# Performance work log

Measured on AMD Instinct MI355X. Metric: run time of the kernel, lower is better.

## Reference

```python
import jax, jax.numpy as jnp
import numpy as np

EMBED_DIM = 128
NUM_HEADS = 16
D_K = EMBED_DIM // NUM_HEADS  # n_wires per head = 8
DEPTH = 1
DIM = 2 ** D_K  # 256 state amplitudes


def _cnot_chain_inverse_perm(d, depth):
    """Inverse permutation of basis states under `depth` rounds of the CNOT ladder
    CNOT(0,1),...,CNOT(d-2,d-1),CNOT(d-1,0). Wire 0 = most significant bit."""
    idx = np.arange(2 ** d)
    shifts = d - 1 - np.arange(d)
    bits = (idx[:, None] >> shifts) & 1  # (2^d, d)
    for _ in range(depth):
        for w in range(d - 1):
            bits[:, w + 1] ^= bits[:, w]
        bits[:, 0] ^= bits[:, d - 1]
    fwd = (bits << shifts).sum(axis=1)  # psi'[fwd[b]] = psi[b]
    inv = np.empty_like(fwd)
    inv[fwd] = idx  # psi'[j] = psi[inv[j]]
    return inv


def _pauliz_signs(d):
    idx = np.arange(2 ** d)
    shifts = d - 1 - np.arange(d)
    bits = (idx[:, None] >> shifts) & 1
    return (1.0 - 2.0 * bits).astype(np.float32)  # (2^d, d)


_INV_PERM = jnp.asarray(_cnot_chain_inverse_perm(D_K, DEPTH))
_SIGNS = jnp.asarray(_pauliz_signs(D_K))


def quantum_head(angles):
    """angles: (..., d) RX rotation angles. Returns PauliZ expectations (..., d).

    Product state amplitudes after per-wire RX from |0..0>: probabilities are
    products of cos^2/sin^2; CNOT ladder is a basis permutation; <Z_w> is a
    signed sum of probabilities."""
    half = angles * 0.5
    c2 = jnp.cos(half) ** 2
    s2 = jnp.sin(half) ** 2
    lead = angles.shape[:-1]
    p = jnp.ones(lead + (1,), angles.dtype)
    for w in range(D_K):  # builds (..., 2^d) probability vector
        pair = jnp.stack([c2[..., w], s2[..., w]], axis=-1)
        p = (p[..., :, None] * pair[..., None, :]).reshape(lead + (-1,))
    p = p[..., _INV_PERM]  # apply CNOT ladder permutation
    return p @ _SIGNS  # (..., d) PauliZ expectations


def setup_inputs() -> dict:
    key = jax.random.key(0)
    ks = jax.random.split(key, 10)
    B, S, E = 8, 512, EMBED_DIM
    sc = 1.0 / np.sqrt(E)
    return {
        "x": jax.random.normal(ks[0], (B, S, E), jnp.float32),
        "Wq": jax.random.normal(ks[1], (E, E), jnp.float32) * sc,
        "bq": jnp.zeros((E,), jnp.float32),
        "Wk": jax.random.normal(ks[2], (E, E), jnp.float32) * sc,
        "bk": jnp.zeros((E,), jnp.float32),
        "Wv": jax.random.normal(ks[3], (E, E), jnp.float32) * sc,
        "bv": jnp.zeros((E,), jnp.float32),
        "Wo": jax.random.normal(ks[4], (E, E), jnp.float32) * sc,
        "bo": jnp.zeros((E,), jnp.float32),
        "theta": jax.random.normal(ks[5], (NUM_HEADS, D_K), jnp.float32),
    }


def reference(x, Wq, bq, Wk, bk, Wv, bv, Wo, bo, theta):
    B, S, E = x.shape
    H, dk = NUM_HEADS, D_K

    def split_heads(y):  # (B,S,E) -> (B,H,S,dk)
        return y.reshape(B, S, H, dk).transpose(0, 2, 1, 3)

    q = split_heads(x @ Wq + bq)
    k = split_heads(x @ Wk + bk)
    v = split_heads(x @ Wv + bv)

    th = theta[None, :, None, :]  # broadcast per-head trainable RX angles
    qh = quantum_head(q + th)
    kh = quantum_head(k + th)
    vh = quantum_head(v + th)

    scores = jnp.einsum("bhsd,bhtd->bhst", qh, kh) / jnp.sqrt(jnp.asarray(dk, x.dtype))
    attn = jax.nn.softmax(scores, axis=-1)
    out = jnp.einsum("bhst,bhtd->bhsd", attn, vh)
    out = out.transpose(0, 2, 1, 3).reshape(B, S, E)
    return out @ Wo + bo
```

## Files before the change

kernel.cpp:

```cpp
#include <hip/hip_runtime.h>
#include <hip/hip_bf16.h>
#include <math.h>

#define BB 8
#define SS 512
#define EE 128
#define HH 16
#define DKK 8

#define FMA4(ACC, S, W) do { (ACC).x += (S)*(W).x; (ACC).y += (S)*(W).y; \
                             (ACC).z += (S)*(W).z; (ACC).w += (S)*(W).w; } while(0)
#define DOT4(A, B) ((A).x*(B).x + (A).y*(B).y + (A).z*(B).z + (A).w*(B).w)

__global__ __launch_bounds__(256, 4) void k_qkvq(
    const float* __restrict__ x,
    const float* __restrict__ Wq, const float* __restrict__ bq,
    const float* __restrict__ Wk, const float* __restrict__ bk,
    const float* __restrict__ Wv, const float* __restrict__ bv,
    const float* __restrict__ theta,
    float* __restrict__ qh, float* __restrict__ kh, float* __restrict__ vh)
{
    __shared__ float xs[16][128];
    const int t = threadIdx.x;
    const int m = blockIdx.y;
    const int row0 = blockIdx.x * 16;

    {
        const float4* xv = (const float4*)(x + (size_t)row0 * 128);
        float4* xsv = (float4*)&xs[0][0];
        xsv[t]       = xv[t];
        xsv[t + 256] = xv[t + 256];
    }
    __syncthreads();

    const int cg   = t & 31;
    const int col0 = cg * 4;
    const int rg   = t >> 5;
    const int r0   = rg * 2;

    const float* __restrict__ W  = (m == 0) ? Wq : (m == 1) ? Wk : Wv;
    const float* __restrict__ bb = (m == 0) ? bq : (m == 1) ? bk : bv;
    float* __restrict__ outp     = (m == 0) ? qh : (m == 1) ? kh : vh;

    float4 acc0 = *(const float4*)&bb[col0];
    float4 acc1 = acc0;

    #pragma unroll 4
    for (int k4 = 0; k4 < 32; ++k4) {
        const float4 xa = ((const float4*)xs[r0 + 0])[k4];
        const float4 xb = ((const float4*)xs[r0 + 1])[k4];
        const float4 w0 = *(const float4*)&W[(k4 * 4 + 0) * 128 + col0];
        const float4 w1 = *(const float4*)&W[(k4 * 4 + 1) * 128 + col0];
        const float4 w2 = *(const float4*)&W[(k4 * 4 + 2) * 128 + col0];
        const float4 w3 = *(const float4*)&W[(k4 * 4 + 3) * 128 + col0];
        FMA4(acc0, xa.x, w0); FMA4(acc0, xa.y, w1);
        FMA4(acc0, xa.z, w2); FMA4(acc0, xa.w, w3);
        FMA4(acc1, xb.x, w0); FMA4(acc1, xb.y, w1);
        FMA4(acc1, xb.z, w2); FMA4(acc1, xb.w, w3);
    }

    const float4 th = *(const float4*)&theta[col0];
    const int h    = cg >> 1;
    const int half = cg & 1;

    float4 accs[2] = {acc0, acc1};
    #pragma unroll
    for (int r = 0; r < 2; ++r) {
        float4 c;
        c.x = __cosf(accs[r].x + th.x);
        c.y = __cosf(accs[r].y + th.y);
        c.z = __cosf(accs[r].z + th.z);
        c.w = __cosf(accs[r].w + th.w);
        const float p0 = c.x;
        const float p1 = p0 * c.y;
        const float p2 = p1 * c.z;
        const float p3 = p2 * c.w;
        const float recv = __shfl_xor(p3, 1);
        float4 o;
        if (half == 0) {
            const float s123 = c.y * c.z * c.w;
            o.x = s123 * recv;
            o.y = p1;
            o.z = p2;
            o.w = p3;
        } else {
            o.x = recv * p0;
            o.y = recv * p1;
            o.z = recv * p2;
            o.w = recv * p3;
        }
        const int g  = row0 + r0 + r;
        const int b_ = g >> 9;
        const int s  = g & 511;
        *(float4*)&outp[(((size_t)b_ * HH + h) * SS + s) * DKK + half * 4] = o;
    }
}

__global__ __launch_bounds__(512, 4) void k_attn(
    const float* __restrict__ qh, const float* __restrict__ kh,
    const float* __restrict__ vh, float* __restrict__ hid)
{
    __shared__ float4 smem[3072];
    float4* kk = smem;
    float4* vv = smem + 1024;

    const int t  = threadIdx.x;
    const int L  = t & 63;
    const int wv = t >> 6;
    const int bh = blockIdx.x & 127;
    const int q0 = (blockIdx.x >> 7) * 256;

    {
        const float4* kg = (const float4*)kh + (size_t)bh * 1024;
        const float4* vg = (const float4*)vh + (size_t)bh * 1024;
        kk[t]       = kg[t];
        kk[t + 512] = kg[t + 512];
        vv[t]       = vg[t];
        vv[t + 512] = vg[t + 512];
    }

    const float scale = 0.35355339059327373f;
    float4 qa[4], qb[4];
    {
        const float4* qg = (const float4*)qh + ((size_t)bh * 512 + q0) * 2;
        #pragma unroll
        for (int r = 0; r < 4; ++r) {
            float4 a = qg[(L + 64 * r) * 2];
            float4 b = qg[(L + 64 * r) * 2 + 1];
            a.x *= scale; a.y *= scale; a.z *= scale; a.w *= scale;
            b.x *= scale; b.y *= scale; b.z *= scale; b.w *= scale;
            qa[r] = a; qb[r] = b;
        }
    }
    __syncthreads();

    float4 aA[4], aB[4];
    float  den[4];
    #pragma unroll
    for (int r = 0; r < 4; ++r) {
        aA[r] = make_float4(0.f, 0.f, 0.f, 0.f);
        aB[r] = make_float4(0.f, 0.f, 0.f, 0.f);
        den[r] = 0.f;
    }

    const float4* kbase = kk + wv * 128;
    const float4* vbase = vv + wv * 128;

    #pragma unroll 4
    for (int j = 0; j < 64; ++j) {
        const float4 k0 = kbase[2 * j];
        const float4 k1 = kbase[2 * j + 1];
        const float4 v0 = vbase[2 * j];
        const float4 v1 = vbase[2 * j + 1];
        #pragma unroll
        for (int r = 0; r < 4; ++r) {
            const float s = DOT4(qa[r], k0) + DOT4(qb[r], k1);
            const float e = __expf(s);
            den[r] += e;
            FMA4(aA[r], e, v0);
            FMA4(aB[r], e, v1);
        }
    }

    __syncthreads();

    float4* part = smem;
    if (wv < 4) {
        #pragma unroll
        for (int r = 0; r < 4; ++r) {
            const int idx = (wv * 256 + L + 64 * r) * 3;
            part[idx]     = aA[r];
            part[idx + 1] = aB[r];
            part[idx + 2] = make_float4(den[r], 0.f, 0.f, 0.f);
        }
    }
    __syncthreads();
    if (wv >= 4) {
        #pragma unroll
        for (int r = 0; r < 4; ++r) {
            const int idx = ((wv - 4) * 256 + L + 64 * r) * 3;
            float4 pa = part[idx];
            float4 pb = part[idx + 1];
            float4 pd = part[idx + 2];
            pa.x += aA[r].x; pa.y += aA[r].y; pa.z += aA[r].z; pa.w += aA[r].w;
            pb.x += aB[r].x; pb.y += aB[r].y; pb.z += aB[r].z; pb.w += aB[r].w;
            pd.x += den[r];
            part[idx]     = pa;
            part[idx + 1] = pb;
            part[idx + 2] = pd;
        }
    }
    __syncthreads();

    if (t < 256) {
        float4 rA = make_float4(0.f, 0.f, 0.f, 0.f), rB = rA;
        float rd = 0.f;
        #pragma unroll
        for (int w = 0; w < 4; ++w) {
            const int idx = (w * 256 + t) * 3;
            const float4 a = part[idx];
            const float4 b = part[idx + 1];
            rA.x += a.x; rA.y += a.y; rA.z += a.z; rA.w += a.w;
            rB.x += b.x; rB.y += b.y; rB.z += b.z; rB.w += b.w;
            rd   += part[idx + 2].x;
        }
        const float inv = 1.0f / rd;
        rA.x *= inv; rA.y *= inv; rA.z *= inv; rA.w *= inv;
        rB.x *= inv; rB.y *= inv; rB.z *= inv; rB.w *= inv;
        const int b_ = bh >> 4, h = bh & 15;
        float* o = hid + ((size_t)(b_ * 512) + q0 + t) * 128 + h * 8;
        ((float4*)o)[0] = rA;
        ((float4*)o)[1] = rB;
    }
}

__global__ __launch_bounds__(256, 4) void k_out(
    const float* __restrict__ hid, const float* __restrict__ Wo,
    const float* __restrict__ bo, float* __restrict__ out)
{
    __shared__ float hs[16][128];
    const int t = threadIdx.x;
    const int row0 = blockIdx.x * 16;

    {
        const float4* hv = (const float4*)(hid + (size_t)row0 * 128);
        float4* hsv = (float4*)&hs[0][0];
        hsv[t]       = hv[t];
        hsv[t + 256] = hv[t + 256];
    }
    __syncthreads();

    const int cg   = t & 31;
    const int col0 = cg * 4;
    const int rg   = t >> 5;
    const int r0   = rg * 2;

    float4 acc0 = *(const float4*)&bo[col0];
    float4 acc1 = acc0;

    #pragma unroll 4
    for (int k4 = 0; k4 < 32; ++k4) {
        const float4 xa = ((const float4*)hs[r0 + 0])[k4];
        const float4 xb = ((const float4*)hs[r0 + 1])[k4];
        const float4 w0 = *(const float4*)&Wo[(k4 * 4 + 0) * 128 + col0];
        const float4 w1 = *(const float4*)&Wo[(k4 * 4 + 1) * 128 + col0];
        const float4 w2 = *(const float4*)&Wo[(k4 * 4 + 2) * 128 + col0];
        const float4 w3 = *(const float4*)&Wo[(k4 * 4 + 3) * 128 + col0];
        FMA4(acc0, xa.x, w0); FMA4(acc0, xa.y, w1);
        FMA4(acc0, xa.z, w2); FMA4(acc0, xa.w, w3);
        FMA4(acc1, xb.x, w0); FMA4(acc1, xb.y, w1);
        FMA4(acc1, xb.z, w2); FMA4(acc1, xb.w, w3);
    }

    *(float4*)&out[(size_t)(row0 + r0 + 0) * 128 + col0] = acc0;
    *(float4*)&out[(size_t)(row0 + r0 + 1) * 128 + col0] = acc1;
}

extern "C" void kernel_launch(void* const* d_in, const int* in_sizes, int n_in,
                              void* d_out, int out_size, void* d_ws, size_t ws_size,
                              hipStream_t stream)
{
    const float* x     = (const float*)d_in[0];
    const float* Wq    = (const float*)d_in[1];
    const float* bq    = (const float*)d_in[2];
    const float* Wk    = (const float*)d_in[3];
    const float* bk    = (const float*)d_in[4];
    const float* Wv    = (const float*)d_in[5];
    const float* bv    = (const float*)d_in[6];
    const float* Wo    = (const float*)d_in[7];
    const float* bo    = (const float*)d_in[8];
    const float* theta = (const float*)d_in[9];
    float* out = (float*)d_out;

    float* ws  = (float*)d_ws;
    float* qh  = ws;
    float* kh  = ws + 524288;
    float* vh  = ws + 1048576;
    float* hid = ws + 1572864;

    k_qkvq<<<dim3(256, 3), 256, 0, stream>>>(x, Wq, bq, Wk, bk, Wv, bv,
                                             theta, qh, kh, vh);
    k_attn<<<256, 512, 0, stream>>>(qh, kh, vh, hid);
    k_out <<<256, 256, 0, stream>>>(hid, Wo, bo, out);
}
```

Measured before the change: 46.01 us.

## Fuse QKV projection and quantum head into attention kernel per (batch, head)

Result: slower. 104.2 us (+126.5%).

```diff
diff --git a/kernel.cpp b/kernel.cpp
--- a/kernel.cpp
+++ b/kernel.cpp
@@ -12,127 +12,134 @@
                              (ACC).z += (S)*(W).z; (ACC).w += (S)*(W).w; } while(0)
 #define DOT4(A, B) ((A).x*(B).x + (A).y*(B).y + (A).z*(B).z + (A).w*(B).w)
 
-__global__ __launch_bounds__(256, 4) void k_qkvq(
+__global__ __launch_bounds__(512, 2) void k_fused(
     const float* __restrict__ x,
     const float* __restrict__ Wq, const float* __restrict__ bq,
     const float* __restrict__ Wk, const float* __restrict__ bk,
     const float* __restrict__ Wv, const float* __restrict__ bv,
     const float* __restrict__ theta,
-    float* __restrict__ qh, float* __restrict__ kh, float* __restrict__ vh)
+    float* __restrict__ hid)
 {
-    __shared__ float xs[16][128];
-    const int t = threadIdx.x;
-    const int m = blockIdx.y;
-    const int row0 = blockIdx.x * 16;
+    __shared__ float smem[12288];
+    float* Kl = smem;
+    float* Vl = smem + 4096;
+    float* ql = smem + 8192;
+
+    const int t   = threadIdx.x;
+    const int bh  = blockIdx.x >> 1;
+    const int qhf = blockIdx.x & 1;
+    const int b_  = bh >> 4;
+    const int h   = bh & 15;
+    const int q0  = qhf * 256;
 
     {
-        const float4* xv = (const float4*)(x + (size_t)row0 * 128);
-        float4* xsv = (float4*)&xs[0][0];
-        xsv[t]       = xv[t];
-        xsv[t + 256] = xv[t + 256];
-    }
-    __syncthreads();
-
-    const int cg   = t & 31;
-    const int col0 = cg * 4;
-    const int rg   = t >> 5;
-    const int r0   = rg * 2;
-
-    const float* __restrict__ W  = (m == 0) ? Wq : (m == 1) ? Wk : Wv;
-    const float* __restrict__ bb = (m == 0) ? bq : (m == 1) ? bk : bv;
-    float* __restrict__ outp     = (m == 0) ? qh : (m == 1) ? kh : vh;
-
-    float4 acc0 = *(const float4*)&bb[col0];
-    float4 acc1 = acc0;
-
-    #pragma unroll 4
-    for (int k4 = 0; k4 < 32; ++k4) {
-        const float4 xa = ((const float4*)xs[r0 + 0])[k4];
-        const float4 xb = ((const float4*)xs[r0 + 1])[k4];
-        const float4 w0 = *(const float4*)&W[(k4 * 4 + 0) * 128 + col0];
-        const float4 w1 = *(const float4*)&W[(k4 * 4 + 1) * 128 + col0];
-        const float4 w2 = *(const float4*)&W[(k4 * 4 + 2) * 128 + col0];
-        const float4 w3 = *(const float4*)&W[(k4 * 4 + 3) * 128 + col0];
-        FMA4(acc0, xa.x, w0); FMA4(acc0, xa.y, w1);
-        FMA4(acc0, xa.z, w2); FMA4(acc0, xa.w, w3);
-        FMA4(acc1, xb.x, w0); FMA4(acc1, xb.y, w1);
-        FMA4(acc1, xb.z, w2); FMA4(acc1, xb.w, w3);
-    }
-
-    const float4 th = *(const float4*)&theta[col0];
-    const int h    = cg >> 1;
-    const int half = cg & 1;
-
-    float4 accs[2] = {acc0, acc1};
-    #pragma unroll
-    for (int r = 0; r < 2; ++r) {
+        const int cg   = t & 3;
+        const int mat  = cg >> 1;
+        const int half = cg & 1;
+        const int col0 = h * 8 + half * 4;
+        const float* __restrict__ W = mat ? Wv : Wk;
+        const float4 bias = *(const float4*)&(mat ? bv : bk)[col0];
+        const float4 th   = *(const float4*)&theta[col0];
+        float* outl = mat ? Vl : Kl;
+        const int rbase = t >> 2;
+
+        for (int round = 0; round < 4; ++round) {
+            const int row = round * 128 + rbase;
+            const float4* xr = (const float4*)(x + ((size_t)b_ * 512 + row) * 128);
+            float4 acc = bias;
+            #pragma unroll 4
+            for (int k4 = 0; k4 < 32; ++k4) {
+                const float4 xv = xr[k4];
+                const float4 w0 = *(const float4*)&W[(k4 * 4 + 0) * 128 + col0];
+                const float4 w1 = *(const float4*)&W[(k4 * 4 + 1) * 128 + col0];
+                const float4 w2 = *(const float4*)&W[(k4 * 4 + 2) * 128 + col0];
+                const float4 w3 = *(const float4*)&W[(k4 * 4 + 3) * 128 + col0];
+                FMA4(acc, xv.x, w0); FMA4(acc, xv.y, w1);
+                FMA4(acc, xv.z, w2); FMA4(acc, xv.w, w3);
+            }
+            float4 c;
+            c.x = __cosf(acc.x + th.x);
+            c.y = __cosf(acc.y + th.y);
+            c.z = __cosf(acc.z + th.z);
+            c.w = __cosf(acc.w + th.w);
+            const float p0 = c.x;
+            const float p1 = p0 * c.y;
+            const float p2 = p1 * c.z;
+            const float p3 = p2 * c.w;
+            const float recv = __shfl_xor(p3, 1);
+            float4 o;
+            if (half == 0) {
+                o.x = c.y * c.z * c.w * recv;
+                o.y = p1;
+                o.z = p2;
+                o.w = p3;
+            } else {
+                o.x = recv * p0;
+                o.y = recv * p1;
+                o.z = recv * p2;
+                o.w = recv * p3;
+            }
+            *(float4*)&outl[row * 8 + half * 4] = o;
+        }
+    }
+
+    {
+        const int cg   = t & 1;
+        const int row  = t >> 1;
+        const int col0 = h * 8 + cg * 4;
+        const float4 bias = *(const float4*)&bq[col0];
+        const float4 th   = *(const float4*)&theta[col0];
+        const float4* xr = (const float4*)(x + ((size_t)b_ * 512 + q0 + row) * 128);
+        float4 acc = bias;
+        #pragma unroll 4
+        for (int k4 = 0; k4 < 32; ++k4) {
+            const float4 xv = xr[k4];
+            const float4 w0 = *(const float4*)&Wq[(k4 * 4 + 0) * 128 + col0];
+            const float4 w1 = *(const float4*)&Wq[(k4 * 4 + 1) * 128 + col0];
+            const float4 w2 = *(const float4*)&Wq[(k4 * 4 + 2) * 128 + col0];
+            const float4 w3 = *(const float4*)&Wq[(k4 * 4 + 3) * 128 + col0];
+            FMA4(acc, xv.x, w0); FMA4(acc, xv.y, w1);
+            FMA4(acc, xv.z, w2); FMA4(acc, xv.w, w3);
+        }
         float4 c;
-        c.x = __cosf(accs[r].x + th.x);
-        c.y = __cosf(accs[r].y + th.y);
-        c.z = __cosf(accs[r].z + th.z);
-        c.w = __cosf(accs[r].w + th.w);
+        c.x = __cosf(acc.x + th.x);
+        c.y = __cosf(acc.y + th.y);
+        c.z = __cosf(acc.z + th.z);
+        c.w = __cosf(acc.w + th.w);
         const float p0 = c.x;
         const float p1 = p0 * c.y;
         const float p2 = p1 * c.z;
         const float p3 = p2 * c.w;
         const float recv = __shfl_xor(p3, 1);
         float4 o;
-        if (half == 0) {
-            const float s123 = c.y * c.z * c.w;
-            o.x = s123 * recv;
-            o.y = p1;
-            o.z = p2;
-            o.w = p3;
+        if (cg == 0) {
+            o.x = c.y * c.z * c.w * recv;
+            o.y = p1; o.z = p2; o.w = p3;
         } else {
-            o.x = recv * p0;
-            o.y = recv * p1;
-            o.z = recv * p2;
-            o.w = recv * p3;
-        }
-        const int g  = row0 + r0 + r;
-        const int b_ = g >> 9;
-        const int s  = g & 511;
-        *(float4*)&outp[(((size_t)b_ * HH + h) * SS + s) * DKK + half * 4] = o;
-    }
-}
-
-__global__ __launch_bounds__(512, 4) void k_attn(
-    const float* __restrict__ qh, const float* __restrict__ kh,
-    const float* __restrict__ vh, float* __restrict__ hid)
-{
-    __shared__ float4 smem[3072];
-    float4* kk = smem;
-    float4* vv = smem + 1024;
-
-    const int t  = threadIdx.x;
+            o.x = recv * p0; o.y = recv * p1;
+            o.z = recv * p2; o.w = recv * p3;
+        }
+        ql[(cg * 4 + 0) * 257 + row] = o.x;
+        ql[(cg * 4 + 1) * 257 + row] = o.y;
+        ql[(cg * 4 + 2) * 257 + row] = o.z;
+        ql[(cg * 4 + 3) * 257 + row] = o.w;
+    }
+    __syncthreads();
+
     const int L  = t & 63;
     const int wv = t >> 6;
-    const int bh = blockIdx.x & 127;
-    const int q0 = (blockIdx.x >> 7) * 256;
-
-    {
-        const float4* kg = (const float4*)kh + (size_t)bh * 1024;
-        const float4* vg = (const float4*)vh + (size_t)bh * 1024;
-        kk[t]       = kg[t];
-        kk[t + 512] = kg[t + 512];
-        vv[t]       = vg[t];
-        vv[t + 512] = vg[t + 512];
-    }
-
-    const float scale = 0.35355339059327373f;
+    const float sc = 0.51012091944f;
+
     float4 qa[4], qb[4];
-    {
-        const float4* qg = (const float4*)qh + ((size_t)bh * 512 + q0) * 2;
-        #pragma unroll
-        for (int r = 0; r < 4; ++r) {
-            float4 a = qg[(L + 64 * r) * 2];
-            float4 b = qg[(L + 64 * r) * 2 + 1];
-            a.x *= scale; a.y *= scale; a.z *= scale; a.w *= scale;
-            b.x *= scale; b.y *= scale; b.z *= scale; b.w *= scale;
-            qa[r] = a; qb[r] = b;
-        }
-    }
-    __syncthreads();
+    #pragma unroll
+    for (int r = 0; r < 4; ++r) {
+        const int row = L + 64 * r;
+        float4 a = make_float4(ql[0*257+row], ql[1*257+row], ql[2*257+row], ql[3*257+row]);
+        float4 b = make_float4(ql[4*257+row], ql[5*257+row], ql[6*257+row], ql[7*257+row]);
+        a.x *= sc; a.y *= sc; a.z *= sc; a.w *= sc;
+        b.x *= sc; b.y *= sc; b.z *= sc; b.w *= sc;
+        qa[r] = a; qb[r] = b;
+    }
 
     float4 aA[4], aB[4];
     float  den[4];
@@ -143,28 +150,27 @@
         den[r] = 0.f;
     }
 
-    const float4* kbase = kk + wv * 128;
-    const float4* vbase = vv + wv * 128;
+    const float* kb = Kl + (wv * 64) * 8;
+    const float* vb = Vl + (wv * 64) * 8;
 
     #pragma unroll 4
     for (int j = 0; j < 64; ++j) {
-        const float4 k0 = kbase[2 * j];
-        const float4 k1 = kbase[2 * j + 1];
-        const float4 v0 = vbase[2 * j];
-        const float4 v1 = vbase[2 * j + 1];
+        const float4 k0 = *(const float4*)&kb[j * 8];
+        const float4 k1 = *(const float4*)&kb[j * 8 + 4];
+        const float4 v0 = *(const float4*)&vb[j * 8];
+        const float4 v1 = *(const float4*)&vb[j * 8 + 4];
         #pragma unroll
         for (int r = 0; r < 4; ++r) {
             const float s = DOT4(qa[r], k0) + DOT4(qb[r], k1);
-            const float e = __expf(s);
+            const float e = exp2f(s);
             den[r] += e;
             FMA4(aA[r], e, v0);
             FMA4(aB[r], e, v1);
         }
     }
-
-    __syncthreads();
-
-    float4* part = smem;
+    __syncthreads();
+
+    float4* part = (float4*)smem;
     if (wv < 4) {
         #pragma unroll
         for (int r = 0; r < 4; ++r) {
@@ -207,7 +213,6 @@
         const float inv = 1.0f / rd;
         rA.x *= inv; rA.y *= inv; rA.z *= inv; rA.w *= inv;
         rB.x *= inv; rB.y *= inv; rB.z *= inv; rB.w *= inv;
-        const int b_ = bh >> 4, h = bh & 15;
         float* o = hid + ((size_t)(b_ * 512) + q0 + t) * 128 + h * 8;
         ((float4*)o)[0] = rA;
         ((float4*)o)[1] = rB;
@@ -272,14 +277,8 @@
     const float* theta = (const float*)d_in[9];
     float* out = (float*)d_out;
 
-    float* ws  = (float*)d_ws;
-    float* qh  = ws;
-    float* kh  = ws + 524288;
-    float* vh  = ws + 1048576;
-    float* hid = ws + 1572864;
-
-    k_qkvq<<<dim3(256, 3), 256, 0, stream>>>(x, Wq, bq, Wk, bk, Wv, bv,
-                                             theta, qh, kh, vh);
-    k_attn<<<256, 512, 0, stream>>>(qh, kh, vh, hid);
-    k_out <<<256, 256, 0, stream>>>(hid, Wo, bo, out);
+    float* hid = (float*)d_ws;
+
+    k_fused<<<256, 512, 0, stream>>>(x, Wq, bq, Wk, bk, Wv, bv, theta, hid);
+    k_out  <<<256, 256, 0, stream>>>(hid, Wo, bo, out);
 }
```

## Split attention over key quarters and fuse partial reduction into output projection

Applied to the files above, without the earlier changes.

Result: slower. 66.25 us (+44.0%).

```diff
diff --git a/kernel.cpp b/kernel.cpp
--- a/kernel.cpp
+++ b/kernel.cpp
@@ -10,6 +10,7 @@
 
 #define FMA4(ACC, S, W) do { (ACC).x += (S)*(W).x; (ACC).y += (S)*(W).y; \
                              (ACC).z += (S)*(W).z; (ACC).w += (S)*(W).w; } while(0)
+#define ADD4(A, B) do { (A).x += (B).x; (A).y += (B).y; (A).z += (B).z; (A).w += (B).w; } while(0)
 #define DOT4(A, B) ((A).x*(B).x + (A).y*(B).y + (A).z*(B).z + (A).w*(B).w)
 
 __global__ __launch_bounds__(256, 4) void k_qkvq(
@@ -78,11 +79,8 @@
         const float recv = __shfl_xor(p3, 1);
         float4 o;
         if (half == 0) {
-            const float s123 = c.y * c.z * c.w;
-            o.x = s123 * recv;
-            o.y = p1;
-            o.z = p2;
-            o.w = p3;
+            o.x = c.y * c.z * c.w * recv;
+            o.y = p1; o.z = p2; o.w = p3;
         } else {
             o.x = recv * p0;
             o.y = recv * p1;
@@ -96,30 +94,28 @@
     }
 }
 
-__global__ __launch_bounds__(512, 4) void k_attn(
+__global__ __launch_bounds__(256, 4) void k_attn(
     const float* __restrict__ qh, const float* __restrict__ kh,
-    const float* __restrict__ vh, float* __restrict__ hid)
-{
-    __shared__ float4 smem[3072];
-    float4* kk = smem;
-    float4* vv = smem + 1024;
-
-    const int t  = threadIdx.x;
-    const int L  = t & 63;
-    const int wv = t >> 6;
-    const int bh = blockIdx.x & 127;
-    const int q0 = (blockIdx.x >> 7) * 256;
+    const float* __restrict__ vh, float* __restrict__ partg)
+{
+    __shared__ float4 smem[1536];
+
+    const int t   = threadIdx.x;
+    const int L   = t & 63;
+    const int wv  = t >> 6;
+    const int bh  = blockIdx.x & 127;
+    const int qhf = (blockIdx.x >> 7) & 1;
+    const int jq  = blockIdx.x >> 8;
+    const int q0  = qhf * 256;
 
     {
-        const float4* kg = (const float4*)kh + (size_t)bh * 1024;
-        const float4* vg = (const float4*)vh + (size_t)bh * 1024;
-        kk[t]       = kg[t];
-        kk[t + 512] = kg[t + 512];
-        vv[t]       = vg[t];
-        vv[t + 512] = vg[t + 512];
-    }
-
-    const float scale = 0.35355339059327373f;
+        const float4* kg = (const float4*)kh + (size_t)bh * 1024 + jq * 256;
+        const float4* vg = (const float4*)vh + (size_t)bh * 1024 + jq * 256;
+        smem[t]       = kg[t];
+        smem[256 + t] = vg[t];
+    }
+
+    const float sc = 0.51012091944f;
     float4 qa[4], qb[4];
     {
         const float4* qg = (const float4*)qh + ((size_t)bh * 512 + q0) * 2;
@@ -127,8 +123,8 @@
         for (int r = 0; r < 4; ++r) {
             float4 a = qg[(L + 64 * r) * 2];
             float4 b = qg[(L + 64 * r) * 2 + 1];
-            a.x *= scale; a.y *= scale; a.z *= scale; a.w *= scale;
-            b.x *= scale; b.y *= scale; b.z *= scale; b.w *= scale;
+            a.x *= sc; a.y *= sc; a.z *= sc; a.w *= sc;
+            b.x *= sc; b.y *= sc; b.z *= sc; b.w *= sc;
             qa[r] = a; qb[r] = b;
         }
     }
@@ -143,11 +139,11 @@
         den[r] = 0.f;
     }
 
-    const float4* kbase = kk + wv * 128;
-    const float4* vbase = vv + wv * 128;
+    const float4* kbase = smem + wv * 64;
+    const float4* vbase = smem + 256 + wv * 64;
 
     #pragma unroll 4
-    for (int j = 0; j < 64; ++j) {
+    for (int j = 0; j < 32; ++j) {
         const float4 k0 = kbase[2 * j];
         const float4 k1 = kbase[2 * j + 1];
         const float4 v0 = vbase[2 * j];
@@ -155,105 +151,104 @@
         #pragma unroll
         for (int r = 0; r < 4; ++r) {
             const float s = DOT4(qa[r], k0) + DOT4(qb[r], k1);
-            const float e = __expf(s);
+            const float e = exp2f(s);
             den[r] += e;
             FMA4(aA[r], e, v0);
             FMA4(aB[r], e, v1);
         }
     }
-
-    __syncthreads();
-
-    float4* part = smem;
-    if (wv < 4) {
+    __syncthreads();
+
+    if (wv < 2) {
         #pragma unroll
         for (int r = 0; r < 4; ++r) {
             const int idx = (wv * 256 + L + 64 * r) * 3;
-            part[idx]     = aA[r];
-            part[idx + 1] = aB[r];
-            part[idx + 2] = make_float4(den[r], 0.f, 0.f, 0.f);
-        }
-    }
-    __syncthreads();
-    if (wv >= 4) {
-        #pragma unroll
-        for (int r = 0; r < 4; ++r) {
-            const int idx = ((wv - 4) * 256 + L + 64 * r) * 3;
-            float4 pa = part[idx];
-            float4 pb = part[idx + 1];
-            float4 pd = part[idx + 2];
-            pa.x += aA[r].x; pa.y += aA[r].y; pa.z += aA[r].z; pa.w += aA[r].w;
-            pb.x += aB[r].x; pb.y += aB[r].y; pb.z += aB[r].z; pb.w += aB[r].w;
-            pd.x += den[r];
-            part[idx]     = pa;
-            part[idx + 1] = pb;
-            part[idx + 2] = pd;
+            smem[idx]     = aA[r];
+            smem[idx + 1] = aB[r];
+            smem[idx + 2] = make_float4(den[r], 0.f, 0.f, 0.f);
+        }
+    }
+    __syncthreads();
+    if (wv >= 2) {
+        #pragma unroll
+        for (int r = 0; r < 4; ++r) {
+            const int idx = ((wv - 2) * 256 + L + 64 * r) * 3;
+            float4 pa = smem[idx];
+            float4 pb = smem[idx + 1];
+            float4 pd = smem[idx + 2];
+            ADD4(pa, aA[r]); ADD4(pb, aB[r]); pd.x += den[r];
+            smem[idx]     = pa;
+            smem[idx + 1] = pb;
+            smem[idx + 2] = pd;
         }
     }
     __syncthreads();
 
     if (t < 256) {
+        const int i0 = t * 3;
+        const int i1 = (256 + t) * 3;
+        float4 rA = smem[i0];     ADD4(rA, smem[i1]);
+        float4 rB = smem[i0 + 1]; ADD4(rB, smem[i1 + 1]);
+        const float rd = smem[i0 + 2].x + smem[i1 + 2].x;
+        float4* gp = (float4*)partg + (((size_t)bh * 4 + jq) * 512 + q0 + t) * 3;
+        gp[0] = rA;
+        gp[1] = rB;
+        gp[2] = make_float4(rd, 0.f, 0.f, 0.f);
+    }
+}
+
+__global__ __launch_bounds__(256, 4) void k_out(
+    const float* __restrict__ partg, const float* __restrict__ Wo,
+    const float* __restrict__ bo, float* __restrict__ out)
+{
+    __shared__ float hs[8][128];
+    const int t = threadIdx.x;
+    const int row0 = blockIdx.x * 8;
+
+    if (t < 128) {
+        const int rt = t >> 4;
+        const int h  = t & 15;
+        const int g  = row0 + rt;
+        const int b_ = g >> 9;
+        const int s  = g & 511;
+        const int bh = b_ * 16 + h;
+        const float4* gp = (const float4*)partg;
         float4 rA = make_float4(0.f, 0.f, 0.f, 0.f), rB = rA;
         float rd = 0.f;
         #pragma unroll
-        for (int w = 0; w < 4; ++w) {
-            const int idx = (w * 256 + t) * 3;
-            const float4 a = part[idx];
-            const float4 b = part[idx + 1];
-            rA.x += a.x; rA.y += a.y; rA.z += a.z; rA.w += a.w;
-            rB.x += b.x; rB.y += b.y; rB.z += b.z; rB.w += b.w;
-            rd   += part[idx + 2].x;
+        for (int jq = 0; jq < 4; ++jq) {
+            const size_t base = (((size_t)bh * 4 + jq) * 512 + s) * 3;
+            float4 a = gp[base];
+            float4 b = gp[base + 1];
+            ADD4(rA, a); ADD4(rB, b);
+            rd += gp[base + 2].x;
         }
         const float inv = 1.0f / rd;
         rA.x *= inv; rA.y *= inv; rA.z *= inv; rA.w *= inv;
         rB.x *= inv; rB.y *= inv; rB.z *= inv; rB.w *= inv;
-        const int b_ = bh >> 4, h = bh & 15;
-        float* o = hid + ((size_t)(b_ * 512) + q0 + t) * 128 + h * 8;
-        ((float4*)o)[0] = rA;
-        ((float4*)o)[1] = rB;
-    }
-}
-
-__global__ __launch_bounds__(256, 4) void k_out(
-    const float* __restrict__ hid, const float* __restrict__ Wo,
-    const float* __restrict__ bo, float* __restrict__ out)
-{
-    __shared__ float hs[16][128];
-    const int t = threadIdx.x;
-    const int row0 = blockIdx.x * 16;
-
-    {
-        const float4* hv = (const float4*)(hid + (size_t)row0 * 128);
-        float4* hsv = (float4*)&hs[0][0];
-        hsv[t]       = hv[t];
-        hsv[t + 256] = hv[t + 256];
+        *(float4*)&hs[rt][h * 8]     = rA;
+        *(float4*)&hs[rt][h * 8 + 4] = rB;
     }
     __syncthreads();
 
     const int cg   = t & 31;
     const int col0 = cg * 4;
     const int rg   = t >> 5;
-    const int r0   = rg * 2;
-
-    float4 acc0 = *(const float4*)&bo[col0];
-    float4 acc1 = acc0;
+
+    float4 acc = *(const float4*)&bo[col0];
 
     #pragma unroll 4
     for (int k4 = 0; k4 < 32; ++k4) {
-        const float4 xa = ((const float4*)hs[r0 + 0])[k4];
-        const float4 xb = ((const float4*)hs[r0 + 1])[k4];
+        const float4 xa = ((const float4*)hs[rg])[k4];
         const float4 w0 = *(const float4*)&Wo[(k4 * 4 + 0) * 128 + col0];
         const float4 w1 = *(const float4*)&Wo[(k4 * 4 + 1) * 128 + col0];
         const float4 w2 = *(const float4*)&Wo[(k4 * 4 + 2) * 128 + col0];
         const float4 w3 = *(const float4*)&Wo[(k4 * 4 + 3) * 128 + col0];
-        FMA4(acc0, xa.x, w0); FMA4(acc0, xa.y, w1);
-        FMA4(acc0, xa.z, w2); FMA4(acc0, xa.w, w3);
-        FMA4(acc1, xb.x, w0); FMA4(acc1, xb.y, w1);
-        FMA4(acc1, xb.z, w2); FMA4(acc1, xb.w, w3);
-    }
-
-    *(float4*)&out[(size_t)(row0 + r0 + 0) * 128 + col0] = acc0;
-    *(float4*)&out[(size_t)(row0 + r0 + 1) * 128 + col0] = acc1;
+        FMA4(acc, xa.x, w0); FMA4(acc, xa.y, w1);
+        FMA4(acc, xa.z, w2); FMA4(acc, xa.w, w3);
+    }
+
+    *(float4*)&out[(size_t)(row0 + rg) * 128 + col0] = acc;
 }
 
 extern "C" void kernel_launch(void* const* d_in, const int* in_sizes, int n_in,
@@ -272,14 +267,14 @@
     const float* theta = (const float*)d_in[9];
     float* out = (float*)d_out;
 
-    float* ws  = (float*)d_ws;
-    float* qh  = ws;
-    float* kh  = ws + 524288;
-    float* vh  = ws + 1048576;
-    float* hid = ws + 1572864;
+    float* ws    = (float*)d_ws;
+    float* qh    = ws;
+    float* kh    = ws + 524288;
+    float* vh    = ws + 1048576;
+    float* partg = ws + 1572864;
 
     k_qkvq<<<dim3(256, 3), 256, 0, stream>>>(x, Wq, bq, Wk, bk, Wv, bv,
                                              theta, qh, kh, vh);
-    k_attn<<<256, 512, 0, stream>>>(qh, kh, vh, hid);
-    k_out <<<256, 256, 0, stream>>>(hid, Wo, bo, out);
-}
+    k_attn<<<1024, 256, 0, stream>>>(qh, kh, vh, partg);
+    k_out <<<512, 256, 0, stream>>>(partg, Wo, bo, out);
+}
```

## Split attention key loop across 16 waves and fold log2e into query scale

Applied to the files above, without the earlier changes.

Result: slower. 66.32 us (+44.1%).

```diff
diff --git a/kernel.cpp b/kernel.cpp
--- a/kernel.cpp
+++ b/kernel.cpp
@@ -10,6 +10,7 @@
 
 #define FMA4(ACC, S, W) do { (ACC).x += (S)*(W).x; (ACC).y += (S)*(W).y; \
                              (ACC).z += (S)*(W).z; (ACC).w += (S)*(W).w; } while(0)
+#define ADD4(A, B) do { (A).x += (B).x; (A).y += (B).y; (A).z += (B).z; (A).w += (B).w; } while(0)
 #define DOT4(A, B) ((A).x*(B).x + (A).y*(B).y + (A).z*(B).z + (A).w*(B).w)
 
 __global__ __launch_bounds__(256, 4) void k_qkvq(
@@ -78,11 +79,8 @@
         const float recv = __shfl_xor(p3, 1);
         float4 o;
         if (half == 0) {
-            const float s123 = c.y * c.z * c.w;
-            o.x = s123 * recv;
-            o.y = p1;
-            o.z = p2;
-            o.w = p3;
+            o.x = c.y * c.z * c.w * recv;
+            o.y = p1; o.z = p2; o.w = p3;
         } else {
             o.x = recv * p0;
             o.y = recv * p1;
@@ -96,13 +94,11 @@
     }
 }
 
-__global__ __launch_bounds__(512, 4) void k_attn(
+__global__ __launch_bounds__(1024, 4) void k_attn(
     const float* __restrict__ qh, const float* __restrict__ kh,
     const float* __restrict__ vh, float* __restrict__ hid)
 {
     __shared__ float4 smem[3072];
-    float4* kk = smem;
-    float4* vv = smem + 1024;
 
     const int t  = threadIdx.x;
     const int L  = t & 63;
@@ -113,13 +109,11 @@
     {
         const float4* kg = (const float4*)kh + (size_t)bh * 1024;
         const float4* vg = (const float4*)vh + (size_t)bh * 1024;
-        kk[t]       = kg[t];
-        kk[t + 512] = kg[t + 512];
-        vv[t]       = vg[t];
-        vv[t + 512] = vg[t + 512];
-    }
-
-    const float scale = 0.35355339059327373f;
+        smem[t]        = kg[t];
+        smem[1024 + t] = vg[t];
+    }
+
+    const float sc = 0.51012091944f;
     float4 qa[4], qb[4];
     {
         const float4* qg = (const float4*)qh + ((size_t)bh * 512 + q0) * 2;
@@ -127,8 +121,8 @@
         for (int r = 0; r < 4; ++r) {
             float4 a = qg[(L + 64 * r) * 2];
             float4 b = qg[(L + 64 * r) * 2 + 1];
-            a.x *= scale; a.y *= scale; a.z *= scale; a.w *= scale;
-            b.x *= scale; b.y *= scale; b.z *= scale; b.w *= scale;
+            a.x *= sc; a.y *= sc; a.z *= sc; a.w *= sc;
+            b.x *= sc; b.y *= sc; b.z *= sc; b.w *= sc;
             qa[r] = a; qb[r] = b;
         }
     }
@@ -143,11 +137,11 @@
         den[r] = 0.f;
     }
 
-    const float4* kbase = kk + wv * 128;
-    const float4* vbase = vv + wv * 128;
+    const float4* kbase = smem + wv * 64;
+    const float4* vbase = smem + 1024 + wv * 64;
 
     #pragma unroll 4
-    for (int j = 0; j < 64; ++j) {
+    for (int j = 0; j < 32; ++j) {
         const float4 k0 = kbase[2 * j];
         const float4 k1 = kbase[2 * j + 1];
         const float4 v0 = vbase[2 * j];
@@ -155,54 +149,53 @@
         #pragma unroll
         for (int r = 0; r < 4; ++r) {
             const float s = DOT4(qa[r], k0) + DOT4(qb[r], k1);
-            const float e = __expf(s);
+            const float e = exp2f(s);
             den[r] += e;
             FMA4(aA[r], e, v0);
             FMA4(aB[r], e, v1);
         }
     }
-
-    __syncthreads();
-
-    float4* part = smem;
+    __syncthreads();
+
     if (wv < 4) {
         #pragma unroll
         for (int r = 0; r < 4; ++r) {
             const int idx = (wv * 256 + L + 64 * r) * 3;
-            part[idx]     = aA[r];
-            part[idx + 1] = aB[r];
-            part[idx + 2] = make_float4(den[r], 0.f, 0.f, 0.f);
-        }
-    }
-    __syncthreads();
-    if (wv >= 4) {
-        #pragma unroll
-        for (int r = 0; r < 4; ++r) {
-            const int idx = ((wv - 4) * 256 + L + 64 * r) * 3;
-            float4 pa = part[idx];
-            float4 pb = part[idx + 1];
-            float4 pd = part[idx + 2];
-            pa.x += aA[r].x; pa.y += aA[r].y; pa.z += aA[r].z; pa.w += aA[r].w;
-            pb.x += aB[r].x; pb.y += aB[r].y; pb.z += aB[r].z; pb.w += aB[r].w;
-            pd.x += den[r];
-            part[idx]     = pa;
-            part[idx + 1] = pb;
-            part[idx + 2] = pd;
-        }
-    }
-    __syncthreads();
+            smem[idx]     = aA[r];
+            smem[idx + 1] = aB[r];
+            smem[idx + 2] = make_float4(den[r], 0.f, 0.f, 0.f);
+        }
+    }
+    __syncthreads();
+    #pragma unroll
+    for (int grp = 1; grp < 4; ++grp) {
+        if ((wv >> 2) == grp) {
+            const int slot = wv & 3;
+            #pragma unroll
+            for (int r = 0; r < 4; ++r) {
+                const int idx = (slot * 256 + L + 64 * r) * 3;
+                float4 pa = smem[idx];
+                float4 pb = smem[idx + 1];
+                float4 pd = smem[idx + 2];
+                ADD4(pa, aA[r]); ADD4(pb, aB[r]); pd.x += den[r];
+                smem[idx]     = pa;
+                smem[idx + 1] = pb;
+                smem[idx + 2] = pd;
+            }
+        }
+        __syncthreads();
+    }
 
     if (t < 256) {
         float4 rA = make_float4(0.f, 0.f, 0.f, 0.f), rB = rA;
         float rd = 0.f;
         #pragma unroll
-        for (int w = 0; w < 4; ++w) {
-            const int idx = (w * 256 + t) * 3;
-            const float4 a = part[idx];
-            const float4 b = part[idx + 1];
-            rA.x += a.x; rA.y += a.y; rA.z += a.z; rA.w += a.w;
-            rB.x += b.x; rB.y += b.y; rB.z += b.z; rB.w += b.w;
-            rd   += part[idx + 2].x;
+        for (int s4 = 0; s4 < 4; ++s4) {
+            const int idx = (s4 * 256 + t) * 3;
+            const float4 a = smem[idx];
+            const float4 b = smem[idx + 1];
+            ADD4(rA, a); ADD4(rB, b);
+            rd += smem[idx + 2].x;
         }
         const float inv = 1.0f / rd;
         rA.x *= inv; rA.y *= inv; rA.z *= inv; rA.w *= inv;
@@ -280,6 +273,6 @@
 
     k_qkvq<<<dim3(256, 3), 256, 0, stream>>>(x, Wq, bq, Wk, bk, Wv, bv,
                                              theta, qh, kh, vh);
-    k_attn<<<256, 512, 0, stream>>>(qh, kh, vh, hid);
+    k_attn<<<256, 1024, 0, stream>>>(qh, kh, vh, hid);
     k_out <<<256, 256, 0, stream>>>(hid, Wo, bo, out);
 }
```
